# Optimization experiments

Hardware: AMD Instinct MI355X
Metric: run time of the kernel (lower is better)

## Reference

```python
import jax, jax.numpy as jnp
import numpy as np

B, D, H, Wd = 8, 64, 256, 256
EMB = 256
NFEAT = 18
NBINS = 16


def setup_inputs() -> dict:
    key = jax.random.key(0)
    k1, k2 = jax.random.split(key, 2)
    volume = jax.random.normal(k1, (B, D, H, Wd), jnp.float32)
    W = jax.random.normal(k2, (NFEAT, EMB), jnp.float32) * 0.1
    b = jnp.zeros((EMB,), jnp.float32)
    gamma = jnp.ones((EMB,), jnp.float32)
    beta = jnp.zeros((EMB,), jnp.float32)
    return {"volume": volume, "W": W, "b": b, "gamma": gamma, "beta": beta}


def _slice_features(sl):
    # sl: [H, W] single slice; mask derived from 80th percentile threshold
    h, w = sl.shape
    flat = sl.reshape(-1)
    npix = flat.shape[0]
    thresh = jnp.quantile(flat, 0.8)  # torch.quantile default: linear interp
    mask = flat >= thresh
    mf = mask.astype(sl.dtype)
    n = mf.sum()  # >= 1 by construction (max always passes)

    mean = (mf * flat).sum() / n
    c = flat - mean
    std = jnp.sqrt((mf * c * c).sum() / n)  # unbiased=False
    std_eps = jnp.maximum(std, 1e-6)
    skew = jnp.clip(((mf * c**3).sum() / n) / std_eps**3, -50.0, 50.0)
    kurt = jnp.clip(((mf * c**4).sum() / n) / std_eps**4, 0.0, 100.0)
    msq = (mf * flat * flat).sum() / n
    absmean = (mf * jnp.abs(flat)).sum() / n

    # sorted masked values: unmasked pushed to +inf end
    big = jnp.finfo(sl.dtype).max
    vs = jnp.sort(jnp.where(mask, flat, big))
    nm1 = n - 1.0
    last = nm1.astype(jnp.int32)

    def quant(p):
        pos = p * nm1
        lo = jnp.floor(pos)
        fr = pos - lo
        lo_i = lo.astype(jnp.int32)
        hi_i = jnp.minimum(lo_i + 1, last)
        return vs[lo_i] * (1.0 - fr) + vs[hi_i] * fr

    q25, q50, q75 = quant(0.25), quant(0.5), quant(0.75)
    vmin = vs[0]
    vmax = vs[last]

    # 16-bin histogram entropy over masked values (torch.histc semantics)
    rng = vmax - vmin
    denom = jnp.where(rng > 0, rng, 1.0)
    bins = jnp.clip(jnp.floor((flat - vmin) / denom * NBINS).astype(jnp.int32), 0, NBINS - 1)
    hist = jnp.zeros((NBINS,), sl.dtype).at[bins].add(mf)
    probs = jnp.maximum(hist / jnp.maximum(hist.sum(), 1.0), 1e-6)
    ent = jnp.where(jnp.isclose(vmin, vmax), 0.0, -(probs * jnp.log(probs)).sum())

    # numpy-style gradient magnitude (central diff interior, one-sided edges)
    gy, gx = jnp.gradient(sl)
    gm = jnp.sqrt(gy * gy + gx * gx).reshape(-1)
    gm_mean = (mf * gm).sum() / n
    gm_std = jnp.sqrt((mf * (gm - gm_mean) ** 2).sum() / n)

    # normalized centroid of the mask
    yi = (jnp.arange(npix) // w).astype(sl.dtype)
    xi = (jnp.arange(npix) % w).astype(sl.dtype)
    cy = (mf * yi).sum() / n / max(h - 1, 1)
    cx = (mf * xi).sum() / n / max(w - 1, 1)

    frac = n / npix  # mask.float().mean() == mask.sum()/numel
    return jnp.stack([mean, std, vmin, vmax, q25, q50, q75, msq, ent,
                      skew, kurt, frac, gm_mean, gm_std, cy, cx, frac, absmean])


def reference(volume, W, b, gamma, beta):
    bsz, depth, h, w = volume.shape
    feats = jax.vmap(_slice_features)(volume.reshape(bsz * depth, h, w))
    feats = feats.reshape(bsz, depth, NFEAT)
    x = feats @ W + b
    mu = x.mean(-1, keepdims=True)
    var = ((x - mu) ** 2).mean(-1, keepdims=True)
    tokens = (x - mu) / jnp.sqrt(var + 1e-5) * gamma + beta
    padding_mask = jnp.zeros((bsz, depth), dtype=bool)
    return tokens, padding_mask
```

## Files before the change

kernel.cpp:

```cpp
#include <hip/hip_runtime.h>
#include <stdint.h>

#define NPIX     65536
#define NTHREADS 1024
#define NSLICES  512
#define NFEAT    18
#define EMB      256
#define THRESH_RANK 52428u
#define NB       24
#define IVMAX    4
#define EPT4     16

__device__ __forceinline__ uint32_t f2key(float f) {
  uint32_t u = __float_as_uint(f);
  return u ^ ((u & 0x80000000u) ? 0xFFFFFFFFu : 0x80000000u);
}
__device__ __forceinline__ float key2f(uint32_t k) {
  uint32_t u = (k & 0x80000000u) ? (k ^ 0x80000000u) : ~k;
  return __uint_as_float(u);
}

__device__ void scan2048(uint32_t* H, uint32_t* Wsum) {
  int tid = threadIdx.x, lane = tid & 63, wid = tid >> 6;
  uint32_t a1 = H[2 * tid + 1];
  uint32_t v = H[2 * tid] + a1;
  for (int d = 1; d < 64; d <<= 1) {
    uint32_t t = __shfl_up(v, d);
    if (lane >= d) v += t;
  }
  if (lane == 63) Wsum[wid] = v;
  __syncthreads();
  uint32_t woff = 0;
  for (int w = 0; w < wid; ++w) woff += Wsum[w];
  v += woff;
  H[2 * tid + 1] = v;
  H[2 * tid]     = v - a1;
  __syncthreads();
}

__device__ __forceinline__ int wfind2048(const uint32_t* C, uint32_t r, int lane) {
  unsigned long long m = __ballot(C[lane * 32 + 31] > r);
  int chunk = __builtin_ctzll(m);
  unsigned long long m2 = __ballot((lane < 32) && (C[chunk * 32 + lane] > r));
  int off = __builtin_ctzll(m2);
  return chunk * 32 + off;
}
__device__ __forceinline__ int wfind256(const uint32_t* P, uint32_t r, int lane) {
  unsigned long long m = __ballot(P[lane * 4 + 3] > r);
  int chunk = __builtin_ctzll(m);
  int off = 0;
  while (off < 3 && P[chunk * 4 + off] <= r) ++off;
  return chunk * 4 + off;
}
__device__ __forceinline__ void wscan256(uint32_t* H, int lane) {
  uint32_t h0 = H[lane * 4 + 0], h1 = H[lane * 4 + 1];
  uint32_t h2 = H[lane * 4 + 2], h3 = H[lane * 4 + 3];
  uint32_t s = h0 + h1 + h2 + h3, inc = s;
  for (int d = 1; d < 64; d <<= 1) { uint32_t o = __shfl_up(inc, d); if (lane >= d) inc += o; }
  uint32_t base = inc - s;
  H[lane * 4 + 0] = base + h0;
  H[lane * 4 + 1] = base + h0 + h1;
  H[lane * 4 + 2] = base + h0 + h1 + h2;
  H[lane * 4 + 3] = base + s;
}

__device__ __forceinline__ int slotOf(uint32_t b, const uint32_t* ivLo, const uint32_t* ivHi,
                                      const uint32_t* ivS0, int niv) {
  for (int j = 0; j < niv; ++j)
    if (b >= ivLo[j] && b <= ivHi[j]) return (int)(ivS0[j] + b - ivLo[j]);
  return -1;
}

__device__ void plan_from_bins(int m, const uint32_t* pbin,
                               uint32_t* ivLo, uint32_t* ivHi, uint32_t* ivS0,
                               int* pniv, int* pnslots) {
  uint32_t b[6];
  for (int i = 0; i < m; ++i) b[i] = pbin[i];
  for (int i = 1; i < m; ++i) {
    uint32_t x = b[i]; int j = i - 1;
    while (j >= 0 && b[j] > x) { b[j + 1] = b[j]; --j; }
    b[j + 1] = x;
  }
  int niv = 0; uint32_t s0 = 0; int i = 0;
  while (i < m && niv < IVMAX) {
    uint32_t lo = b[i], hi = b[i]; ++i;
    while (i < m && b[i] <= hi + 1) { hi = max(hi, b[i]); ++i; }
    ivLo[niv] = lo; ivHi[niv] = hi; ivS0[niv] = s0;
    s0 += hi - lo + 1; ++niv;
  }
  for (int j = niv; j < IVMAX; ++j) { ivLo[j] = 0xFFFFu; ivHi[j] = 0u; ivS0[j] = 0u; }
  *pniv = niv; *pnslots = (int)s0;
}

__global__ __launch_bounds__(NTHREADS) void feat_kernel(const float* __restrict__ vol,
                                                        float* __restrict__ feats) {
  __shared__ uint32_t HC1[2048];
  __shared__ uint32_t L2H[NB * 256];
  __shared__ uint32_t Wsum[16];
  __shared__ double   tmpD9[16 * 9];
  __shared__ double   s_red[9];
  __shared__ uint32_t H16[16 * 16];
  __shared__ uint32_t smaxkey;
  __shared__ uint32_t s_ivLo[IVMAX], s_ivHi[IVMAX], s_ivS0[IVMAX];
  __shared__ int      s_niv, s_nslots;
  __shared__ float    s_thresh;
  __shared__ uint32_t s_cnlt;
  __shared__ float    s_qA[3], s_qB[3], s_qfr[3];
  __shared__ int      s_qdup[3];
  __shared__ uint32_t s_prank[6], s_pbin[6];
  __shared__ uint8_t  s_ptag[6];
  __shared__ int      s_npend;

  const int tid  = threadIdx.x;
  const int lane = tid & 63;
  const int wid  = tid >> 6;
  const float*  sl  = vol + (size_t)blockIdx.x * NPIX;
  const float4* sl4 = (const float4*)sl;

  HC1[2 * tid] = 0; HC1[2 * tid + 1] = 0;
  if (tid == 0) smaxkey = 0u;
  if (tid < 256) H16[tid] = 0u;
  __syncthreads();
  uint32_t mk = 0u;
#pragma unroll 4
  for (int t = 0; t < EPT4; ++t) {
    float4 f = sl4[tid + t * NTHREADS];
    uint32_t k0 = f2key(f.x), k1 = f2key(f.y), k2 = f2key(f.z), k3 = f2key(f.w);
    mk = max(mk, max(max(k0, k1), max(k2, k3)));
    atomicAdd(&HC1[k0 >> 21], 1u);
    atomicAdd(&HC1[k1 >> 21], 1u);
    atomicAdd(&HC1[k2 >> 21], 1u);
    atomicAdd(&HC1[k3 >> 21], 1u);
  }
  for (int d = 32; d > 0; d >>= 1) { uint32_t o = __shfl_down(mk, d); mk = max(mk, o); }
  if (lane == 0) atomicMax(&smaxkey, mk);
  __syncthreads();
  scan2048(HC1, Wsum);

  if (tid < 64) {
    int b1t = wfind2048(HC1, THRESH_RANK, lane);
    uint32_t clo  = b1t ? HC1[b1t - 1] : 0u;
    uint32_t cmax = min(THRESH_RANK, HC1[b1t] - 1u);
    uint32_t rl[4], rh[4];
    rl[0] = (uint32_t)b1t; rh[0] = (uint32_t)b1t;
    const float pp[3] = {0.25f, 0.5f, 0.75f};
#pragma unroll
    for (int qi = 0; qi < 3; ++qi) {
      float p = pp[qi];
      uint32_t rlo = clo  + (uint32_t)(int)floorf(p * ((float)(NPIX - clo)  - 1.0f));
      uint32_t rhi = cmax + (uint32_t)(int)floorf(p * ((float)(NPIX - cmax) - 1.0f)) + 1u;
      if (rhi > NPIX - 1u) rhi = NPIX - 1u;
      if (rlo > rhi) rlo = rhi;
      uint32_t ba = (uint32_t)wfind2048(HC1, rlo, lane);
      uint32_t bb = (uint32_t)wfind2048(HC1, rhi, lane);
      if (bb > ba + 5u) bb = ba + 5u;
      rl[qi + 1] = ba; rh[qi + 1] = bb;
    }
    if (lane == 0) {
      for (int i = 1; i < 4; ++i) {
        uint32_t xl = rl[i], xh = rh[i]; int j = i - 1;
        while (j >= 0 && rl[j] > xl) { rl[j + 1] = rl[j]; rh[j + 1] = rh[j]; --j; }
        rl[j + 1] = xl; rh[j + 1] = xh;
      }
      int niv = 0; uint32_t s0 = 0; int i = 0;
      while (i < 4 && niv < IVMAX && s0 < NB) {
        uint32_t lo = rl[i], hi = rh[i]; ++i;
        while (i < 4 && rl[i] <= hi + 1u) { hi = max(hi, rh[i]); ++i; }
        uint32_t cnt = hi - lo + 1u;
        if (s0 + cnt > NB) { cnt = NB - s0; hi = lo + cnt - 1u; }
        s_ivLo[niv] = lo; s_ivHi[niv] = hi; s_ivS0[niv] = s0;
        s0 += cnt; ++niv;
      }
      for (int j = niv; j < IVMAX; ++j) { s_ivLo[j] = 0xFFFFu; s_ivHi[j] = 0u; s_ivS0[j] = 0u; }
      s_niv = niv; s_nslots = (int)s0;
    }
  }
  __syncthreads();

  for (int round = 0; round < 4; ++round) {
    {
      int ns = s_nslots;
      for (int i = tid; i < ns * 256; i += NTHREADS) L2H[i] = 0u;
    }
    __syncthreads();
    {
      uint32_t lo0 = s_ivLo[0], hi0 = s_ivHi[0], s00 = s_ivS0[0];
      uint32_t lo1 = s_ivLo[1], hi1 = s_ivHi[1], s01 = s_ivS0[1];
      uint32_t lo2 = s_ivLo[2], hi2 = s_ivHi[2], s02 = s_ivS0[2];
      uint32_t lo3 = s_ivLo[3], hi3 = s_ivHi[3], s03 = s_ivS0[3];
#pragma unroll 4
      for (int t = 0; t < EPT4; ++t) {
        float4 f = sl4[tid + t * NTHREADS];
#define PB(vv)                                                                  \
        { uint32_t k = f2key(vv); uint32_t b = k >> 21; uint32_t l2 = (k >> 13) & 255u; \
          if      (b >= lo0 && b <= hi0) atomicAdd(&L2H[(s00 + b - lo0) * 256 + l2], 1u); \
          else if (b >= lo1 && b <= hi1) atomicAdd(&L2H[(s01 + b - lo1) * 256 + l2], 1u); \
          else if (b >= lo2 && b <= hi2) atomicAdd(&L2H[(s02 + b - lo2) * 256 + l2], 1u); \
          else if (b >= lo3 && b <= hi3) atomicAdd(&L2H[(s03 + b - lo3) * 256 + l2], 1u); }
        PB(f.x) PB(f.y) PB(f.z) PB(f.w)
#undef PB
      }
    }
    __syncthreads();
    {
      int ns = s_nslots;
      for (int s = wid; s < ns; s += 16) wscan256(&L2H[s * 256], lane);
    }
    __syncthreads();

    if (tid < 64) {
      int niv = s_niv;
      if (round == 0) {
        int b1t = wfind2048(HC1, THRESH_RANK, lane);
        uint32_t below = b1t ? HC1[b1t - 1] : 0u;
        int sl_ = slotOf((uint32_t)b1t, s_ivLo, s_ivHi, s_ivS0, niv);
        const uint32_t* P = &L2H[sl_ * 256];
        int b2 = wfind256(P, THRESH_RANK - below, lane);
        uint32_t cnlt = below + (b2 ? P[b2 - 1] : 0u);
        float th = key2f(((uint32_t)b1t << 21) | ((uint32_t)b2 << 13));
        if (lane == 0) { s_thresh = th; s_cnlt = cnlt; }
        uint32_t n = NPIX - cnlt, t0 = cnlt;
        float nm1f = (float)n - 1.0f;
        int last = (int)nm1f;
        const float pp[3] = {0.25f, 0.5f, 0.75f};
        int np = 0;
        for (int qi = 0; qi < 3; ++qi) {
          float pos = pp[qi] * nm1f;
          float lof = floorf(pos);
          float fr = pos - lof;
          int lo_i = (int)lof;
          int hi_i = min(lo_i + 1, last);
          bool needB = (fr > 0.0f) && (hi_i != lo_i);
          if (lane == 0) { s_qfr[qi] = fr; s_qdup[qi] = needB ? 0 : 1; }
          {
            uint32_t r = t0 + (uint32_t)lo_i;
            int b = wfind2048(HC1, r, lane);
            uint32_t bw = b ? HC1[b - 1] : 0u;
            int sq = slotOf((uint32_t)b, s_ivLo, s_ivHi, s_ivS0, niv);
            if (sq >= 0) {
              const uint32_t* Pq = &L2H[sq * 256];
              int b2q = wfind256(Pq, r - bw, lane);
              float v = key2f(((uint32_t)b << 21) | ((uint32_t)b2q << 13));
              if (lane == 0) { s_qA[qi] = v; s_qB[qi] = v; }
            } else {
              if (lane == 0) { s_prank[np] = r; s_ptag[np] = (uint8_t)(qi * 2); s_pbin[np] = (uint32_t)b; }
              ++np;
            }
          }
          if (needB) {
            uint32_t r = t0 + (uint32_t)hi_i;
            int b = wfind2048(HC1, r, lane);
            uint32_t bw = b ? HC1[b - 1] : 0u;
            int sq = slotOf((uint32_t)b, s_ivLo, s_ivHi, s_ivS0, niv);
            if (sq >= 0) {
              const uint32_t* Pq = &L2H[sq * 256];
              int b2q = wfind256(Pq, r - bw, lane);
              float v = key2f(((uint32_t)b << 21) | ((uint32_t)b2q << 13));
              if (lane == 0) s_qB[qi] = v;
            } else {
              if (lane == 0) { s_prank[np] = r; s_ptag[np] = (uint8_t)(qi * 2 + 1); s_pbin[np] = (uint32_t)b; }
              ++np;
            }
          }
        }
        if (lane == 0) {
          s_npend = np;
          if (np > 0) plan_from_bins(np, s_pbin, s_ivLo, s_ivHi, s_ivS0, &s_niv, &s_nslots);
        }
      } else {
        int np = s_npend, newnp = 0;
        for (int i = 0; i < np; ++i) {
          uint32_t r = s_prank[i];
          int tg = s_ptag[i];
          int b = wfind2048(HC1, r, lane);
          uint32_t bw = b ? HC1[b - 1] : 0u;
          int sq = slotOf((uint32_t)b, s_ivLo, s_ivHi, s_ivS0, niv);
          if (sq >= 0) {
            const uint32_t* Pq = &L2H[sq * 256];
            int b2q = wfind256(Pq, r - bw, lane);
            float v = key2f(((uint32_t)b << 21) | ((uint32_t)b2q << 13));
            if (lane == 0) { if (tg & 1) s_qB[tg >> 1] = v; else s_qA[tg >> 1] = v; }
          } else {
            if (lane == 0) { s_prank[newnp] = r; s_ptag[newnp] = (uint8_t)tg; s_pbin[newnp] = (uint32_t)b; }
            ++newnp;
          }
        }
        if (lane == 0) {
          s_npend = newnp;
          if (newnp > 0) plan_from_bins(newnp, s_pbin, s_ivLo, s_ivHi, s_ivS0, &s_niv, &s_nslots);
        }
      }
    }
    __syncthreads();
    if (s_npend == 0) break;
    __syncthreads();
  }

  const float thresh = s_thresh;
  const uint32_t n = NPIX - s_cnlt;
  const float vmax  = key2f(smaxkey);
  const float vminf = thresh;

  float rng = vmax - vminf;
  float denomf = (rng > 0.0f) ? rng : 1.0f;
  float sxl = 0, sx2l = 0, sx3l = 0, sx4l = 0, sabl = 0, sgl = 0, sg2l = 0;
  uint32_t syi = 0, sxi = 0;
#pragma unroll 4
  for (int t = 0; t < EPT4; ++t) {
    int i4 = tid + t * NTHREADS;
    float4 v = sl4[i4];
    bool m0 = v.x >= thresh, m1 = v.y >= thresh, m2 = v.z >= thresh, m3 = v.w >= thresh;
    if (m0 | m1 | m2 | m3) {
      int y = i4 >> 6, xb = (i4 & 63) << 2;
      float4 up = sl4[(y > 0)   ? (i4 - 64) : i4];
      float4 dn = sl4[(y < 255) ? (i4 + 64) : i4];
      float lf = (xb > 0)   ? sl[4 * i4 - 1] : 0.0f;
      float rt = (xb < 252) ? sl[4 * i4 + 4] : 0.0f;
#define DOC(mc, vc, upc, dnc, lv, rv, xc)                                      \
      if (mc) {                                                                \
        float gy = (y == 0) ? (dnc - vc) : ((y == 255) ? (vc - upc) : 0.5f * (dnc - upc)); \
        int xx = xb + (xc);                                                    \
        float gx = (xx == 0) ? (rv - vc) : ((xx == 255) ? (vc - lv) : 0.5f * (rv - lv));   \
        float gm = sqrtf(gy * gy + gx * gx);                                   \
        sgl += gm; sg2l += gm * gm;                                            \
        float v2 = vc * vc;                                                    \
        sxl += vc; sx2l += v2; sx3l += v2 * vc; sx4l += v2 * v2;               \
        sabl += fabsf(vc);                                                     \
        syi += (uint32_t)y; sxi += (uint32_t)xx;                               \
        float bf = floorf((vc - vminf) / denomf * 16.0f);                      \
        int bin = (int)bf; bin = bin < 0 ? 0 : (bin > 15 ? 15 : bin);          \
        atomicAdd(&H16[(wid << 4) + bin], 1u);                                 \
      }
      DOC(m0, v.x, up.x, dn.x, lf,  v.y, 0)
      DOC(m1, v.y, up.y, dn.y, v.x, v.z, 1)
      DOC(m2, v.z, up.z, dn.z, v.y, v.w, 2)
      DOC(m3, v.w, up.w, dn.w, v.z, rt,  3)
#undef DOC
    }
  }

  double a[9] = {(double)sxl, (double)sx2l, (double)sx3l, (double)sx4l,
                 (double)sabl, (double)sgl, (double)sg2l, (double)syi, (double)sxi};
#pragma unroll
  for (int k = 0; k < 9; ++k)
    for (int d = 32; d > 0; d >>= 1) a[k] += __shfl_down(a[k], d);
  if (lane == 0) {
#pragma unroll
    for (int k = 0; k < 9; ++k) tmpD9[wid * 9 + k] = a[k];
  }
  __syncthreads();
  if (tid < 64) {
    double r0 = 0, r1 = 0, r2 = 0, r3 = 0, r4 = 0, r5 = 0, r6 = 0, r7 = 0, r8 = 0;
    if (lane < 16) {
      r0 = tmpD9[lane * 9 + 0]; r1 = tmpD9[lane * 9 + 1]; r2 = tmpD9[lane * 9 + 2];
      r3 = tmpD9[lane * 9 + 3]; r4 = tmpD9[lane * 9 + 4]; r5 = tmpD9[lane * 9 + 5];
      r6 = tmpD9[lane * 9 + 6]; r7 = tmpD9[lane * 9 + 7]; r8 = tmpD9[lane * 9 + 8];
    }
    for (int d = 8; d > 0; d >>= 1) {
      r0 += __shfl_down(r0, d); r1 += __shfl_down(r1, d); r2 += __shfl_down(r2, d);
      r3 += __shfl_down(r3, d); r4 += __shfl_down(r4, d); r5 += __shfl_down(r5, d);
      r6 += __shfl_down(r6, d); r7 += __shfl_down(r7, d); r8 += __shfl_down(r8, d);
    }
    if (lane == 0) {
      s_red[0] = r0; s_red[1] = r1; s_red[2] = r2; s_red[3] = r3; s_red[4] = r4;
      s_red[5] = r5; s_red[6] = r6; s_red[7] = r7; s_red[8] = r8;
    }
  }
  __syncthreads();

  if (tid == 0) {
    double sx = s_red[0], sx2 = s_red[1], sx3 = s_red[2], sx4 = s_red[3];
    double sab = s_red[4], sg = s_red[5], sg2 = s_red[6], syid = s_red[7], sxid = s_red[8];
    double dn = (double)n;
    double mean = sx / dn;
    double M2 = sx2 - sx * sx / dn;
    double std_ = sqrt(M2 / dn);
    double se = fmax(std_, 1e-6);
    double S3 = sx3 - 3.0 * mean * sx2 + 2.0 * dn * mean * mean * mean;
    double S4 = sx4 - 4.0 * mean * sx3 + 6.0 * mean * mean * sx2
                - 3.0 * dn * mean * mean * mean * mean;
    double skew = (S3 / dn) / (se * se * se);
    skew = fmin(fmax(skew, -50.0), 50.0);
    double kurt = (S4 / dn) / (se * se * se * se);
    kurt = fmin(fmax(kurt, 0.0), 100.0);
    double msq = sx2 / dn;
    double absmean = sab / dn;

    double ent = 0.0;
    double nden = fmax(dn, 1.0);
    for (int bi = 0; bi < 16; ++bi) {
      uint32_t hb = 0;
#pragma unroll
      for (int w = 0; w < 16; ++w) hb += H16[(w << 4) + bi];
      double p = fmax((double)hb / nden, 1e-6);
      ent -= p * log(p);
    }
    if (fabsf(vminf - vmax) <= 1e-8f + 1e-5f * fabsf(vmax)) ent = 0.0;

    double gmean = sg / dn;
    double gstd = sqrt(fmax(sg2 / dn - gmean * gmean, 0.0));
    double cy = (syid / dn) / 255.0;
    double cx = (sxid / dn) / 255.0;
    double frac = dn / (double)NPIX;

    float qv[3];
#pragma unroll
    for (int qi = 0; qi < 3; ++qi) {
      float A = s_qA[qi];
      float Bv = s_qdup[qi] ? A : s_qB[qi];
      float fr = s_qfr[qi];
      qv[qi] = A * (1.0f - fr) + Bv * fr;
    }

    float* fo = feats + (size_t)blockIdx.x * NFEAT;
    fo[0]  = (float)mean;  fo[1]  = (float)std_;  fo[2]  = vminf;       fo[3]  = vmax;
    fo[4]  = qv[0];        fo[5]  = qv[1];        fo[6]  = qv[2];       fo[7]  = (float)msq;
    fo[8]  = (float)ent;   fo[9]  = (float)skew;  fo[10] = (float)kurt; fo[11] = (float)frac;
    fo[12] = (float)gmean; fo[13] = (float)gstd;  fo[14] = (float)cy;   fo[15] = (float)cx;
    fo[16] = (float)frac;  fo[17] = (float)absmean;
  }
}

__global__ __launch_bounds__(EMB) void token_kernel(const float* __restrict__ feats,
                                                    const float* __restrict__ W,
                                                    const float* __restrict__ b,
                                                    const float* __restrict__ gamma,
                                                    const float* __restrict__ beta,
                                                    float* __restrict__ out,
                                                    float* __restrict__ maskout) {
  __shared__ float f[NFEAT];
  __shared__ float red[4];
  int s = blockIdx.x, e = threadIdx.x;
  if (e < NFEAT) f[e] = feats[(size_t)s * NFEAT + e];
  __syncthreads();
  float acc = b[e];
#pragma unroll
  for (int k = 0; k < NFEAT; ++k) acc += f[k] * W[k * EMB + e];
  int lane = e & 63, wd = e >> 6;
  float sum = acc;
  for (int d = 32; d > 0; d >>= 1) sum += __shfl_down(sum, d);
  if (lane == 0) red[wd] = sum;
  __syncthreads();
  float mu = (red[0] + red[1] + red[2] + red[3]) * (1.0f / EMB);
  float c = acc - mu;
  float s2 = c * c;
  for (int d = 32; d > 0; d >>= 1) s2 += __shfl_down(s2, d);
  __syncthreads();
  if (lane == 0) red[wd] = s2;
  __syncthreads();
  float var = (red[0] + red[1] + red[2] + red[3]) * (1.0f / EMB);
  float o = c / sqrtf(var + 1e-5f) * gamma[e] + beta[e];
  out[(size_t)s * EMB + e] = o;
  if (e == 0) maskout[s] = 0.0f;
}

extern "C" void kernel_launch(void* const* d_in, const int* in_sizes, int n_in,
                              void* d_out, int out_size, void* d_ws, size_t ws_size,
                              hipStream_t stream) {
  const float* vol   = (const float*)d_in[0];
  const float* W     = (const float*)d_in[1];
  const float* b     = (const float*)d_in[2];
  const float* gamma = (const float*)d_in[3];
  const float* beta  = (const float*)d_in[4];
  float* out = (float*)d_out;
  float* feats = (float*)d_ws;

  feat_kernel<<<NSLICES, NTHREADS, 0, stream>>>(vol, feats);
  token_kernel<<<NSLICES, EMB, 0, stream>>>(feats, W, b, gamma, beta,
                                            out, out + (size_t)NSLICES * EMB);
}
```

Baseline: 111.2 us.

## Stream rows per wavefront with register reuse for gradient stencil

The masked-moment loop is restructured so each wavefront walks 16 consecutive image rows. Each lane keeps up/cur/down float4 rows in registers, and left/right neighbours come from lane shuffles instead of extra shared/global loads. The per-element branching is replaced with mask-multiplied FMAs, and the histogram division becomes a multiply by a precomputed reciprocal. f2key is made branchless. Every pixel now computes a sqrt and moments even when unmasked, trading extra ALU work for fewer loads and less divergence, and the reciprocal could shift a bin at a boundary.

```diff
diff --git a/kernel.cpp b/kernel.cpp
--- a/kernel.cpp
+++ b/kernel.cpp
@@ -13,7 +13,7 @@
 
 __device__ __forceinline__ uint32_t f2key(float f) {
   uint32_t u = __float_as_uint(f);
-  return u ^ ((u & 0x80000000u) ? 0xFFFFFFFFu : 0x80000000u);
+  return u ^ ((uint32_t)((int32_t)u >> 31) | 0x80000000u);
 }
 __device__ __forceinline__ float key2f(uint32_t k) {
   uint32_t u = (k & 0x80000000u) ? (k ^ 0x80000000u) : ~k;
@@ -303,39 +303,54 @@
 
   float rng = vmax - vminf;
   float denomf = (rng > 0.0f) ? rng : 1.0f;
+  float sc16 = 16.0f / denomf;
   float sxl = 0, sx2l = 0, sx3l = 0, sx4l = 0, sabl = 0, sgl = 0, sg2l = 0;
   uint32_t syi = 0, sxi = 0;
-#pragma unroll 4
-  for (int t = 0; t < EPT4; ++t) {
-    int i4 = tid + t * NTHREADS;
-    float4 v = sl4[i4];
-    bool m0 = v.x >= thresh, m1 = v.y >= thresh, m2 = v.z >= thresh, m3 = v.w >= thresh;
-    if (m0 | m1 | m2 | m3) {
-      int y = i4 >> 6, xb = (i4 & 63) << 2;
-      float4 up = sl4[(y > 0)   ? (i4 - 64) : i4];
-      float4 dn = sl4[(y < 255) ? (i4 + 64) : i4];
-      float lf = (xb > 0)   ? sl[4 * i4 - 1] : 0.0f;
-      float rt = (xb < 252) ? sl[4 * i4 + 4] : 0.0f;
-#define DOC(mc, vc, upc, dnc, lv, rv, xc)                                      \
-      if (mc) {                                                                \
-        float gy = (y == 0) ? (dnc - vc) : ((y == 255) ? (vc - upc) : 0.5f * (dnc - upc)); \
-        int xx = xb + (xc);                                                    \
-        float gx = (xx == 0) ? (rv - vc) : ((xx == 255) ? (vc - lv) : 0.5f * (rv - lv));   \
-        float gm = sqrtf(gy * gy + gx * gx);                                   \
-        sgl += gm; sg2l += gm * gm;                                            \
-        float v2 = vc * vc;                                                    \
-        sxl += vc; sx2l += v2; sx3l += v2 * vc; sx4l += v2 * v2;               \
-        sabl += fabsf(vc);                                                     \
-        syi += (uint32_t)y; sxi += (uint32_t)xx;                               \
-        float bf = floorf((vc - vminf) / denomf * 16.0f);                      \
-        int bin = (int)bf; bin = bin < 0 ? 0 : (bin > 15 ? 15 : bin);          \
-        atomicAdd(&H16[(wid << 4) + bin], 1u);                                 \
-      }
-      DOC(m0, v.x, up.x, dn.x, lf,  v.y, 0)
-      DOC(m1, v.y, up.y, dn.y, v.x, v.z, 1)
-      DOC(m2, v.z, up.z, dn.z, v.y, v.w, 2)
-      DOC(m3, v.w, up.w, dn.w, v.z, rt,  3)
+  {
+    const int y0 = wid * 16;
+    float4 cur = sl4[y0 * 64 + lane];
+    float4 up  = (y0 > 0) ? sl4[(y0 - 1) * 64 + lane] : cur;
+    float4 dn  = sl4[(y0 + 1) * 64 + lane];
+#pragma unroll
+    for (int r = 0; r < 16; ++r) {
+      const int y = y0 + r;
+      float4 nx = (y + 2 <= 255) ? sl4[(y + 2) * 64 + lane] : dn;
+      float lf = __shfl_up(cur.w, 1);
+      float rt = __shfl_down(cur.x, 1);
+      float gy0, gy1, gy2, gy3;
+      if (y == 0)        { gy0 = dn.x - cur.x; gy1 = dn.y - cur.y; gy2 = dn.z - cur.z; gy3 = dn.w - cur.w; }
+      else if (y == 255) { gy0 = cur.x - up.x; gy1 = cur.y - up.y; gy2 = cur.z - up.z; gy3 = cur.w - up.w; }
+      else { gy0 = 0.5f * (dn.x - up.x); gy1 = 0.5f * (dn.y - up.y);
+             gy2 = 0.5f * (dn.z - up.z); gy3 = 0.5f * (dn.w - up.w); }
+      float gx0 = (lane == 0)  ? (cur.y - cur.x) : 0.5f * (cur.y - lf);
+      float gx1 = 0.5f * (cur.z - cur.x);
+      float gx2 = 0.5f * (cur.w - cur.y);
+      float gx3 = (lane == 63) ? (cur.w - cur.z) : 0.5f * (rt - cur.z);
+#define DOC(vc, gyc, gxc, xc)                                                  \
+      { bool mc = (vc) >= thresh;                                              \
+        float mm = mc ? 1.0f : 0.0f;                                           \
+        float gm = sqrtf((gyc) * (gyc) + (gxc) * (gxc));                       \
+        sgl  = fmaf(mm, gm, sgl);                                              \
+        sg2l = fmaf(mm * gm, gm, sg2l);                                        \
+        float v2 = (vc) * (vc);                                                \
+        sxl  = fmaf(mm, (vc), sxl);                                            \
+        sx2l = fmaf(mm, v2, sx2l);                                             \
+        sx3l = fmaf(mm * v2, (vc), sx3l);                                      \
+        sx4l = fmaf(mm * v2, v2, sx4l);                                        \
+        sabl = fmaf(mm, fabsf(vc), sabl);                                      \
+        syi += mc ? (uint32_t)y : 0u;                                          \
+        sxi += mc ? (uint32_t)((lane << 2) + (xc)) : 0u;                       \
+        if (mc) {                                                              \
+          float bf = floorf(((vc) - vminf) * sc16);                            \
+          int bin = (int)bf; bin = bin < 0 ? 0 : (bin > 15 ? 15 : bin);        \
+          atomicAdd(&H16[(wid << 4) + bin], 1u);                               \
+        } }
+      DOC(cur.x, gy0, gx0, 0)
+      DOC(cur.y, gy1, gx1, 1)
+      DOC(cur.z, gy2, gx2, 2)
+      DOC(cur.w, gy3, gx3, 3)
 #undef DOC
+      up = cur; cur = dn; dn = nx;
     }
   }
 
```

After: 149.3 us. +34.3%, slower.
